# Performance work log

Hardware: AMD Instinct MI355X
Metric: run time of the kernel (lower is better)

## Reference

```python
import jax, jax.numpy as jnp
import numpy as np

B, N, D, P = 512, 64, 256, 512   # graphs, nodes/graph, feat dim, pairs/graph
DEG = 16
E = B * N * DEG                  # 524288 edges
H = 512                          # classifier hidden dim
LR_OUT, CR_OUT, MR_OUT = 4, 6, 17


def setup_inputs() -> dict:
    key = jax.random.key(0)
    ks = jax.random.split(key, 20)
    x = jax.random.normal(ks[0], (B * N, D), jnp.float32)
    # edges stay within each graph, as in a collated batch of graphs
    offs_e = jnp.repeat(jnp.arange(B, dtype=jnp.int32) * N, N * DEG)
    src = jax.random.randint(ks[1], (E,), 0, N, dtype=jnp.int32) + offs_e
    dst = jax.random.randint(ks[2], (E,), 0, N, dtype=jnp.int32) + offs_e
    edge_index = jnp.stack([src, dst])
    pairs = jax.random.randint(ks[3], (B, P, 2), 0, N, dtype=jnp.int32)
    s = 0.02
    inp = {
        'x': x, 'edge_index': edge_index, 'pairs': pairs,
        'gcn_w1': jax.random.normal(ks[4], (D, D), jnp.float32) * s,
        'gcn_b1': jnp.zeros((D,), jnp.float32),
        'gcn_w2': jax.random.normal(ks[5], (D, D), jnp.float32) * s,
        'gcn_b2': jnp.zeros((D,), jnp.float32),
        'lr_w1': jax.random.normal(ks[6], (D, H), jnp.float32) * s,
        'lr_b1': jnp.zeros((H,), jnp.float32),
        'lr_w2': jax.random.normal(ks[7], (H, LR_OUT), jnp.float32) * s,
        'lr_b2': jnp.zeros((LR_OUT,), jnp.float32),
        'cr_w1': jax.random.normal(ks[8], (D, H), jnp.float32) * s,
        'cr_b1': jnp.zeros((H,), jnp.float32),
        'cr_w2': jax.random.normal(ks[9], (H, CR_OUT), jnp.float32) * s,
        'cr_b2': jnp.zeros((CR_OUT,), jnp.float32),
        'mr_w1': jax.random.normal(ks[10], (D, H), jnp.float32) * s,
        'mr_b1': jnp.zeros((H,), jnp.float32),
        'mr_w2': jax.random.normal(ks[11], (H, MR_OUT), jnp.float32) * s,
        'mr_b2': jnp.zeros((MR_OUT,), jnp.float32),
    }
    return inp


def _gcn(x, src, dst, gcn_w1, gcn_b1, gcn_w2, gcn_b2):
    # vanilla GCN with self-loops and symmetric normalization
    n_tot = x.shape[0]
    loops = jnp.arange(n_tot, dtype=src.dtype)
    s = jnp.concatenate([src, loops])
    d = jnp.concatenate([dst, loops])
    deg = jax.ops.segment_sum(jnp.ones_like(s, dtype=x.dtype), d, num_segments=n_tot)
    norm = jax.lax.rsqrt(deg[s] * deg[d])  # [E + n_tot]

    def layer(h, W, b, act):
        m = jax.ops.segment_sum(h[s] * norm[:, None], d, num_segments=n_tot)
        o = m @ W + b
        return jax.nn.relu(o) if act else o

    h = layer(x, gcn_w1, gcn_b1, True)
    return layer(h, gcn_w2, gcn_b2, False)


def _mlp(z, w1, b1, w2, b2):
    return jax.nn.relu(z @ w1 + b1) @ w2 + b2


def reference(x, edge_index, pairs,
              gcn_w1, gcn_b1, gcn_w2, gcn_b2,
              lr_w1, lr_b1, lr_w2, lr_b2,
              cr_w1, cr_b1, cr_w2, cr_b2,
              mr_w1, mr_b1, mr_w2, mr_b2):
    emb = _gcn(x, edge_index[0], edge_index[1], gcn_w1, gcn_b1, gcn_w2, gcn_b2)  # [B*N, D]
    # decollate + batched pair gather (replaces the python double loop)
    offs = (jnp.arange(B, dtype=pairs.dtype) * N)[:, None, None]  # [B,1,1]
    gp = pairs + offs                                            # global node ids [B,P,2]
    e0 = emb[gp[..., 0].reshape(-1)].reshape(B, P, D)
    e1 = emb[gp[..., 1].reshape(-1)].reshape(B, P, D)
    ci = 0.5 * (e0 + e1)  # aggregate(emb0, emb1, 'mean')
    lr = _mlp(ci, lr_w1, lr_b1, lr_w2, lr_b2)
    cr = _mlp(ci, cr_w1, cr_b1, cr_w2, cr_b2)
    mr = _mlp(ci, mr_w1, mr_b1, mr_w2, mr_b2)
    return (lr, cr, mr)
```

## Files before the change

kernel.cpp:

```cpp
#include <hip/hip_runtime.h>
#include <hip/hip_bf16.h>

typedef __bf16 bf16x8 __attribute__((ext_vector_type(8)));
typedef __bf16 bf16x4 __attribute__((ext_vector_type(4)));
typedef float f32x16 __attribute__((ext_vector_type(16)));
typedef unsigned short u16x8 __attribute__((ext_vector_type(8)));
typedef unsigned int u32x4 __attribute__((ext_vector_type(4)));

#define E_EDGES 524288
#define OUT_CR_OFF 1048576
#define OUT_MR_OFF 2621440

static __device__ __forceinline__ float bf2f_(unsigned short u) {
  unsigned int x = ((unsigned int)u) << 16;
  return __builtin_bit_cast(float, x);
}
static __device__ __forceinline__ unsigned short f2bf_(float f) {
  return __builtin_bit_cast(unsigned short, (__bf16)f);
}
static __device__ __forceinline__ unsigned int pack2_(float a, float b) {
  return ((unsigned int)f2bf_(b) << 16) | (unsigned int)f2bf_(a);
}

__global__ void pack_weights(const float* __restrict__ lw1, const float* __restrict__ cw1,
                             const float* __restrict__ mw1,
                             const float* __restrict__ lw2, const float* __restrict__ cw2,
                             const float* __restrict__ mw2,
                             unsigned short* __restrict__ w1tp,
                             unsigned short* __restrict__ w2tp) {
  int idx = blockIdx.x * 256 + threadIdx.x;
  const int n1 = 3 * 16 * 32 * 32 * 8;
  if (idx < n1) {
    int h = idx >> 17;
    int rem = idx & 131071;
    int t = rem >> 13;
    int rem2 = rem & 8191;
    int kc = rem2 >> 8;
    int rem3 = rem2 & 255;
    int hidl = rem3 >> 3;
    int j = rem3 & 7;
    const float* w1 = (h == 0) ? lw1 : (h == 1) ? cw1 : mw1;
    w1tp[idx] = f2bf_(w1[(kc * 8 + j) * 512 + t * 32 + hidl]);
  } else {
    int i2 = idx - n1;
    if (i2 < 3 * 64 * 32 * 8) {
      int h = i2 >> 14;
      int rem = i2 & 16383;
      int kc = rem >> 8;
      int rem2 = rem & 255;
      int o = rem2 >> 3;
      int j = rem2 & 7;
      const float* w2 = (h == 0) ? lw2 : (h == 1) ? cw2 : mw2;
      int OUTD = (h == 0) ? 4 : (h == 1) ? 6 : 17;
      w2tp[i2] = (o < OUTD) ? f2bf_(w2[(kc * 8 + j) * OUTD + o]) : (unsigned short)0;
    }
  }
}

template <bool PACKED>
__launch_bounds__(512, 2)
__global__ void fused_gcn_heads(
    const float* __restrict__ x,
    const int* __restrict__ esrc, const int* __restrict__ edst,
    const int* __restrict__ pairs,
    const float* __restrict__ gw1, const float* __restrict__ gb1,
    const float* __restrict__ gw2, const float* __restrict__ gb2,
    const float* __restrict__ lw1, const float* __restrict__ lb1,
    const float* __restrict__ lw2, const float* __restrict__ lb2,
    const float* __restrict__ cw1, const float* __restrict__ cb1,
    const float* __restrict__ cw2, const float* __restrict__ cb2,
    const float* __restrict__ mw1, const float* __restrict__ mb1,
    const float* __restrict__ mw2, const float* __restrict__ mb2,
    const unsigned short* __restrict__ w1tp,
    const unsigned short* __restrict__ w2tp,
    float* __restrict__ out) {
  __shared__ unsigned short bufM[64 * 256];
  __shared__ __align__(16) unsigned short w1tile[8192];
  __shared__ __align__(16) unsigned short w2tile[1024];
  __shared__ float b1s[512];
  __shared__ __align__(16) short eS[1024], eD[1024];
  __shared__ short csr[1024];
  __shared__ int csroff[65];
  __shared__ float invdeg[64], rdeg[64];

  const int b = blockIdx.x, tid = threadIdx.x;
  const int wv = tid >> 6, lane = tid & 63;

  {
    const float4* xg = (const float4*)(x + b * (64 * 256));
    for (int i = tid; i < 4096; i += 512) {
      float4 v = xg[i];
      ushort4 o;
      o.x = f2bf_(v.x); o.y = f2bf_(v.y); o.z = f2bf_(v.z); o.w = f2bf_(v.w);
      *(ushort4*)&bufM[i * 4] = o;
    }
    const int eb = b * 1024, nb = b * 64;
    for (int i = tid; i < 1024; i += 512) {
      eS[i] = (short)(esrc[eb + i] - nb);
      eD[i] = (short)(edst[eb + i] - nb);
    }
  }
  __syncthreads();

  if (tid < 64) {
    const short n = (short)tid;
    int cnt = 0;
    for (int c = 0; c < 128; ++c) {
      const u16x8 dv = *(const u16x8*)&eD[c * 8];
#pragma unroll
      for (int j = 0; j < 8; ++j) cnt += ((short)dv[j] == n) ? 1 : 0;
    }
    int val = cnt;
#pragma unroll
    for (int off = 1; off < 64; off <<= 1) {
      int up = __shfl_up(val, off, 64);
      if (tid >= off) val += up;
    }
    csroff[tid] = val - cnt;
    if (tid == 63) csroff[64] = val;
    const float dg = (float)(cnt + 1);
    invdeg[tid] = 1.0f / dg;
    rdeg[tid] = rsqrtf(dg);
    int pos = val - cnt;
    for (int c = 0; c < 128; ++c) {
      const u16x8 dv = *(const u16x8*)&eD[c * 8];
      const u16x8 sv = *(const u16x8*)&eS[c * 8];
#pragma unroll
      for (int j = 0; j < 8; ++j)
        if ((short)dv[j] == n) csr[pos++] = (short)sv[j];
    }
  }
  __syncthreads();

  float4 acc[8];

  auto do_agg = [&]() {
#pragma unroll
    for (int k = 0; k < 8; ++k) {
      const int n = wv * 8 + k;
      const ushort4 xv = *(const ushort4*)&bufM[n * 256 + lane * 4];
      const float sd = invdeg[n];
      float ax = bf2f_(xv.x) * sd, ay = bf2f_(xv.y) * sd;
      float az = bf2f_(xv.z) * sd, aw = bf2f_(xv.w) * sd;
      const float rn = rdeg[n];
      const int eb0 = csroff[n], eb1 = csroff[n + 1];
      for (int e = eb0; e < eb1; ++e) {
        const int s = csr[e];
        const float wgt = rn * rdeg[s];
        const ushort4 sv = *(const ushort4*)&bufM[s * 256 + lane * 4];
        ax += bf2f_(sv.x) * wgt; ay += bf2f_(sv.y) * wgt;
        az += bf2f_(sv.z) * wgt; aw += bf2f_(sv.w) * wgt;
      }
      acc[k].x = ax; acc[k].y = ay; acc[k].z = az; acc[k].w = aw;
    }
  };

  auto writeback = [&]() {
#pragma unroll
    for (int k = 0; k < 8; ++k) {
      const int n = wv * 8 + k;
      ushort4 o;
      o.x = f2bf_(acc[k].x); o.y = f2bf_(acc[k].y);
      o.z = f2bf_(acc[k].z); o.w = f2bf_(acc[k].w);
      *(ushort4*)&bufM[n * 256 + lane * 4] = o;
    }
  };

  auto do_matmul = [&](const float* __restrict__ W, const float* __restrict__ bias,
                       bool relu) {
#pragma unroll
    for (int k = 0; k < 8; ++k) { acc[k].x = 0.f; acc[k].y = 0.f; acc[k].z = 0.f; acc[k].w = 0.f; }
    for (int d0 = 0; d0 < 256; d0 += 8) {
      float4 wr[8];
#pragma unroll
      for (int r = 0; r < 8; ++r) wr[r] = ((const float4*)(W + (d0 + r) * 256))[lane];
#pragma unroll
      for (int k = 0; k < 8; ++k) {
        const int n = wv * 8 + k;
        const u16x8 m8 = *(const u16x8*)&bufM[n * 256 + d0];
#pragma unroll
        for (int r = 0; r < 8; ++r) {
          const float s = bf2f_(m8[r]);
          acc[k].x += wr[r].x * s; acc[k].y += wr[r].y * s;
          acc[k].z += wr[r].z * s; acc[k].w += wr[r].w * s;
        }
      }
    }
    const float4 bb = ((const float4*)bias)[lane];
#pragma unroll
    for (int k = 0; k < 8; ++k) {
      acc[k].x += bb.x; acc[k].y += bb.y; acc[k].z += bb.z; acc[k].w += bb.w;
      if (relu) {
        acc[k].x = fmaxf(acc[k].x, 0.f); acc[k].y = fmaxf(acc[k].y, 0.f);
        acc[k].z = fmaxf(acc[k].z, 0.f); acc[k].w = fmaxf(acc[k].w, 0.f);
      }
    }
  };

  do_agg();
  __syncthreads(); writeback(); __syncthreads();
  do_matmul(gw1, gb1, true);
  __syncthreads(); writeback(); __syncthreads();
  do_agg();
  __syncthreads(); writeback(); __syncthreads();
  do_matmul(gw2, gb2, false);
  __syncthreads(); writeback(); __syncthreads();

  const int half = lane >> 5, ln = lane & 31;

  bf16x8 ci[2][16];
#pragma unroll
  for (int pg = 0; pg < 2; ++pg) {
    const int p = wv * 64 + pg * 32 + ln;
    const int2 pr = ((const int2*)pairs)[b * 512 + p];
    const unsigned short* e0 = &bufM[pr.x * 256];
    const unsigned short* e1 = &bufM[pr.y * 256];
#pragma unroll
    for (int s = 0; s < 16; ++s) {
      const int ko = s * 16 + half * 8;
      const u16x8 r0 = *(const u16x8*)(e0 + ko);
      const u16x8 r1 = *(const u16x8*)(e1 + ko);
      bf16x8 v;
#pragma unroll
      for (int j = 0; j < 8; ++j) v[j] = (__bf16)(0.5f * (bf2f_(r0[j]) + bf2f_(r1[j])));
      ci[pg][s] = v;
    }
  }

  for (int h = 0; h < 3; ++h) {
    const float* w1p = (h == 0) ? lw1 : (h == 1) ? cw1 : mw1;
    const float* w2p = (h == 0) ? lw2 : (h == 1) ? cw2 : mw2;
    const float* b1p = (h == 0) ? lb1 : (h == 1) ? cb1 : mb1;
    const float* b2p = (h == 0) ? lb2 : (h == 1) ? cb2 : mb2;
    const int OUTD = (h == 0) ? 4 : (h == 1) ? 6 : 17;
    float* outp = out + ((h == 0) ? 0 : (h == 1) ? OUT_CR_OFF : OUT_MR_OFF);

    __syncthreads();
    b1s[tid] = b1p[tid];

    f32x16 acc2[2];
#pragma unroll
    for (int i = 0; i < 16; ++i) { acc2[0][i] = 0.f; acc2[1][i] = 0.f; }

    for (int t = 0; t < 16; ++t) {
      __syncthreads();
      if (PACKED) {
        const float4* g1 = ((const float4*)w1tp) + (h * 16 + t) * 1024;
        float4* d1 = (float4*)w1tile;
        d1[tid] = g1[tid];
        d1[tid + 512] = g1[tid + 512];
        if (tid < 128)
          ((float4*)w2tile)[tid] = ((const float4*)w2tp)[(h * 64 + t * 4) * 32 + tid];
      } else {
        const int hidl = tid & 31, kc2 = tid >> 5;
#pragma unroll
        for (int r = 0; r < 2; ++r) {
          const int kc = kc2 * 2 + r;
          bf16x8 v;
#pragma unroll
          for (int j = 0; j < 8; ++j)
            v[j] = (__bf16)w1p[(kc * 8 + j) * 512 + t * 32 + hidl];
          *(bf16x8*)&w1tile[(kc * 32 + hidl) * 8] = v;
        }
        if (tid < 256) {
          const int q = tid >> 6, rem = tid & 63, o = rem >> 1, jh = rem & 1;
          bf16x4 v;
#pragma unroll
          for (int jj = 0; jj < 4; ++jj) {
            const int row = (t * 4 + q) * 8 + jh * 4 + jj;
            v[jj] = (o < OUTD) ? (__bf16)w2p[row * OUTD + o] : (__bf16)0.f;
          }
          *(bf16x4*)&w2tile[(q * 32 + o) * 8 + jh * 4] = v;
        }
      }
      __syncthreads();

#pragma unroll
      for (int pg = 0; pg < 2; ++pg) {
        f32x16 acc1;
#pragma unroll
        for (int i = 0; i < 16; ++i) acc1[i] = 0.f;
#pragma unroll
        for (int s = 0; s < 16; ++s) {
          const bf16x8 a = *(const bf16x8*)&w1tile[((2 * s + half) * 32 + ln) * 8];
          acc1 = __builtin_amdgcn_mfma_f32_32x32x16_bf16(a, ci[pg][s], acc1, 0, 0, 0);
        }
        float hv[16];
#pragma unroll
        for (int i = 0; i < 16; ++i) {
          const int row = (i & 3) + 8 * (i >> 2) + 4 * half;
          hv[i] = fmaxf(acc1[i] + b1s[t * 32 + row], 0.f);
        }
#pragma unroll
        for (int ks = 0; ks < 2; ++ks) {
          const int bse = ks * 8;
          const unsigned x0 = pack2_(hv[bse + 0], hv[bse + 1]);
          const unsigned x1 = pack2_(hv[bse + 2], hv[bse + 3]);
          const unsigned y0 = pack2_(hv[bse + 4], hv[bse + 5]);
          const unsigned y1 = pack2_(hv[bse + 6], hv[bse + 7]);
          const unsigned px0 = __shfl_xor(x0, 32);
          const unsigned px1 = __shfl_xor(x1, 32);
          const unsigned py0 = __shfl_xor(y0, 32);
          const unsigned py1 = __shfl_xor(y1, 32);
          u32x4 wt;
          wt[0] = half ? py0 : x0;
          wt[1] = half ? py1 : x1;
          wt[2] = half ? y0 : px0;
          wt[3] = half ? y1 : px1;
          const bf16x8 bfrag = __builtin_bit_cast(bf16x8, wt);
          const bf16x8 a2 = *(const bf16x8*)&w2tile[((ks * 2 + half) * 32 + ln) * 8];
          acc2[pg] = __builtin_amdgcn_mfma_f32_32x32x16_bf16(a2, bfrag, acc2[pg], 0, 0, 0);
        }
      }
    }

#pragma unroll
    for (int pg = 0; pg < 2; ++pg) {
      const int p = wv * 64 + pg * 32 + ln;
      const long q = (long)b * 512 + p;
#pragma unroll
      for (int g4 = 0; g4 < 4; ++g4) {
        const int o0 = g4 * 8 + 4 * half;
#pragma unroll
        for (int e = 0; e < 4; ++e) {
          const int o = o0 + e;
          if (o < OUTD) outp[q * OUTD + o] = acc2[pg][g4 * 4 + e] + b2p[o];
        }
      }
    }
  }
}

extern "C" void kernel_launch(void* const* d_in, const int* in_sizes, int n_in,
                              void* d_out, int out_size, void* d_ws, size_t ws_size,
                              hipStream_t stream) {
  (void)in_sizes; (void)n_in; (void)out_size;
  const float* x   = (const float*)d_in[0];
  const int* eidx  = (const int*)d_in[1];
  const int* pairs = (const int*)d_in[2];
  const float* gw1 = (const float*)d_in[3];
  const float* gb1 = (const float*)d_in[4];
  const float* gw2 = (const float*)d_in[5];
  const float* gb2 = (const float*)d_in[6];
  const float* lw1 = (const float*)d_in[7];
  const float* lb1 = (const float*)d_in[8];
  const float* lw2 = (const float*)d_in[9];
  const float* lb2 = (const float*)d_in[10];
  const float* cw1 = (const float*)d_in[11];
  const float* cb1 = (const float*)d_in[12];
  const float* cw2 = (const float*)d_in[13];
  const float* cb2 = (const float*)d_in[14];
  const float* mw1 = (const float*)d_in[15];
  const float* mb1 = (const float*)d_in[16];
  const float* mw2 = (const float*)d_in[17];
  const float* mb2 = (const float*)d_in[18];

  const size_t NEED = (size_t)(3 * 16 * 32 * 32 * 8 + 3 * 64 * 32 * 8) * 2;
  unsigned short* w1tp = (unsigned short*)d_ws;
  unsigned short* w2tp = w1tp + 3 * 16 * 32 * 32 * 8;

  if (d_ws != nullptr && ws_size >= NEED) {
    pack_weights<<<1728, 256, 0, stream>>>(lw1, cw1, mw1, lw2, cw2, mw2, w1tp, w2tp);
    fused_gcn_heads<true><<<512, 512, 0, stream>>>(
        x, eidx, eidx + E_EDGES, pairs, gw1, gb1, gw2, gb2,
        lw1, lb1, lw2, lb2, cw1, cb1, cw2, cb2, mw1, mb1, mw2, mb2,
        w1tp, w2tp, (float*)d_out);
  } else {
    fused_gcn_heads<false><<<512, 512, 0, stream>>>(
        x, eidx, eidx + E_EDGES, pairs, gw1, gb1, gw2, gb2,
        lw1, lb1, lw2, lb2, cw1, cb1, cw2, cb2, mw1, mb1, mw2, mb2,
        w1tp, w2tp, (float*)d_out);
  }
}
```

Baseline: 509.4 us.

## Use MFMA for GCN matmuls, swizzle LDS, double-buffer head weight tiles

The two GCN layer matmuls move from scalar FP32 FMA loops over global weights to bf16 MFMA, using a new pre-packed GCN weight layout in the workspace. Node features in LDS are stored with an XOR swizzle to reduce bank conflicts. The head MLP loop is flattened over all 48 head/tile steps, with a double-buffered LDS weight tile whose global loads are issued before the current tile's compute, and one barrier per step. Adds an LDS union and setprio hints; the GCN matmul now rounds weights to bf16, a precision change.

```diff
diff --git a/kernel.cpp b/kernel.cpp
--- a/kernel.cpp
+++ b/kernel.cpp
@@ -10,6 +10,9 @@
 #define E_EDGES 524288
 #define OUT_CR_OFF 1048576
 #define OUT_MR_OFF 2621440
+#define W1TP_ELEMS (48 * 9216)
+#define GCNW_ELEMS (2 * 8 * 16 * 64 * 8)
+#define WS_NEED ((size_t)(W1TP_ELEMS + GCNW_ELEMS) * 2)
 
 static __device__ __forceinline__ float bf2f_(unsigned short u) {
   unsigned int x = ((unsigned int)u) << 16;
@@ -22,37 +25,38 @@
   return ((unsigned int)f2bf_(b) << 16) | (unsigned int)f2bf_(a);
 }
 
-__global__ void pack_weights(const float* __restrict__ lw1, const float* __restrict__ cw1,
+__global__ void pack_weights(const float* __restrict__ gw1, const float* __restrict__ gw2,
+                             const float* __restrict__ lw1, const float* __restrict__ cw1,
                              const float* __restrict__ mw1,
                              const float* __restrict__ lw2, const float* __restrict__ cw2,
                              const float* __restrict__ mw2,
                              unsigned short* __restrict__ w1tp,
-                             unsigned short* __restrict__ w2tp) {
-  int idx = blockIdx.x * 256 + threadIdx.x;
-  const int n1 = 3 * 16 * 32 * 32 * 8;
-  if (idx < n1) {
-    int h = idx >> 17;
-    int rem = idx & 131071;
-    int t = rem >> 13;
-    int rem2 = rem & 8191;
-    int kc = rem2 >> 8;
-    int rem3 = rem2 & 255;
-    int hidl = rem3 >> 3;
-    int j = rem3 & 7;
-    const float* w1 = (h == 0) ? lw1 : (h == 1) ? cw1 : mw1;
-    w1tp[idx] = f2bf_(w1[(kc * 8 + j) * 512 + t * 32 + hidl]);
+                             unsigned short* __restrict__ gcnw) {
+  const int idx = blockIdx.x * 256 + threadIdx.x;
+  if (idx < W1TP_ELEMS) {
+    const int ht = idx / 9216;
+    const int r = idx - ht * 9216;
+    const int h = ht >> 4, tt = ht & 15;
+    if (r < 8192) {
+      const int kc = r >> 8, r2 = r & 255, hidl = r2 >> 3, j = r2 & 7;
+      const float* w1 = (h == 0) ? lw1 : (h == 1) ? cw1 : mw1;
+      w1tp[idx] = f2bf_(w1[(kc * 8 + j) * 512 + tt * 32 + hidl]);
+    } else {
+      const int r2 = r - 8192;
+      const int q = r2 >> 8, r3 = r2 & 255, o = r3 >> 3, j = r3 & 7;
+      const float* w2 = (h == 0) ? lw2 : (h == 1) ? cw2 : mw2;
+      const int OUTD = (h == 0) ? 4 : (h == 1) ? 6 : 17;
+      w1tp[idx] = (o < OUTD) ? f2bf_(w2[((tt * 4 + q) * 8 + j) * OUTD + o])
+                             : (unsigned short)0;
+    }
   } else {
-    int i2 = idx - n1;
-    if (i2 < 3 * 64 * 32 * 8) {
-      int h = i2 >> 14;
-      int rem = i2 & 16383;
-      int kc = rem >> 8;
-      int rem2 = rem & 255;
-      int o = rem2 >> 3;
-      int j = rem2 & 7;
-      const float* w2 = (h == 0) ? lw2 : (h == 1) ? cw2 : mw2;
-      int OUTD = (h == 0) ? 4 : (h == 1) ? 6 : 17;
-      w2tp[i2] = (o < OUTD) ? f2bf_(w2[(kc * 8 + j) * OUTD + o]) : (unsigned short)0;
+    const int g = idx - W1TP_ELEMS;
+    if (g < GCNW_ELEMS) {
+      const int layer = g >> 16, r = g & 65535;
+      const int O = r >> 13, r2 = r & 8191, s = r2 >> 9;
+      const int r3 = r2 & 511, lane = r3 >> 3, j = r3 & 7;
+      const float* W = layer ? gw2 : gw1;
+      gcnw[g] = f2bf_(W[(s * 16 + (lane >> 5) * 8 + j) * 256 + O * 32 + (lane & 31)]);
     }
   }
 }
@@ -72,32 +76,37 @@
     const float* __restrict__ mw1, const float* __restrict__ mb1,
     const float* __restrict__ mw2, const float* __restrict__ mb2,
     const unsigned short* __restrict__ w1tp,
-    const unsigned short* __restrict__ w2tp,
+    const unsigned short* __restrict__ gcnw,
     float* __restrict__ out) {
-  __shared__ unsigned short bufM[64 * 256];
-  __shared__ __align__(16) unsigned short w1tile[8192];
-  __shared__ __align__(16) unsigned short w2tile[1024];
-  __shared__ float b1s[512];
-  __shared__ __align__(16) short eS[1024], eD[1024];
-  __shared__ short csr[1024];
+  __shared__ unsigned short bufM[16384];
+  __shared__ union WU {
+    struct GG { short eS[1024]; short eD[1024]; short csr[1024]; } g;
+    unsigned short wbuf[2][9216];
+  } U;
   __shared__ int csroff[65];
   __shared__ float invdeg[64], rdeg[64];
+  __shared__ float b1s[1568];
 
   const int b = blockIdx.x, tid = threadIdx.x;
   const int wv = tid >> 6, lane = tid & 63;
+  const int half = lane >> 5, ln = lane & 31;
+
+  auto sidx = [](int node, int boff) {
+    return (node * 512 + (boff ^ ((node & 15) << 4))) >> 1;
+  };
 
   {
-    const float4* xg = (const float4*)(x + b * (64 * 256));
+    const float4* xg = (const float4*)(x + b * 16384);
     for (int i = tid; i < 4096; i += 512) {
-      float4 v = xg[i];
-      ushort4 o;
-      o.x = f2bf_(v.x); o.y = f2bf_(v.y); o.z = f2bf_(v.z); o.w = f2bf_(v.w);
-      *(ushort4*)&bufM[i * 4] = o;
+      const float4 v = xg[i];
+      ushort4 o4;
+      o4.x = f2bf_(v.x); o4.y = f2bf_(v.y); o4.z = f2bf_(v.z); o4.w = f2bf_(v.w);
+      *(ushort4*)&bufM[sidx(i >> 6, (i & 63) * 8)] = o4;
     }
     const int eb = b * 1024, nb = b * 64;
     for (int i = tid; i < 1024; i += 512) {
-      eS[i] = (short)(esrc[eb + i] - nb);
-      eD[i] = (short)(edst[eb + i] - nb);
+      U.g.eS[i] = (short)(esrc[eb + i] - nb);
+      U.g.eD[i] = (short)(edst[eb + i] - nb);
     }
   }
   __syncthreads();
@@ -106,14 +115,14 @@
     const short n = (short)tid;
     int cnt = 0;
     for (int c = 0; c < 128; ++c) {
-      const u16x8 dv = *(const u16x8*)&eD[c * 8];
+      const u16x8 dv = *(const u16x8*)&U.g.eD[c * 8];
 #pragma unroll
       for (int j = 0; j < 8; ++j) cnt += ((short)dv[j] == n) ? 1 : 0;
     }
     int val = cnt;
 #pragma unroll
     for (int off = 1; off < 64; off <<= 1) {
-      int up = __shfl_up(val, off, 64);
+      const int up = __shfl_up(val, off, 64);
       if (tid >= off) val += up;
     }
     csroff[tid] = val - cnt;
@@ -123,11 +132,11 @@
     rdeg[tid] = rsqrtf(dg);
     int pos = val - cnt;
     for (int c = 0; c < 128; ++c) {
-      const u16x8 dv = *(const u16x8*)&eD[c * 8];
-      const u16x8 sv = *(const u16x8*)&eS[c * 8];
+      const u16x8 dv = *(const u16x8*)&U.g.eD[c * 8];
+      const u16x8 sv = *(const u16x8*)&U.g.eS[c * 8];
 #pragma unroll
       for (int j = 0; j < 8; ++j)
-        if ((short)dv[j] == n) csr[pos++] = (short)sv[j];
+        if ((short)dv[j] == n) U.g.csr[pos++] = (short)sv[j];
     }
   }
   __syncthreads();
@@ -138,16 +147,16 @@
 #pragma unroll
     for (int k = 0; k < 8; ++k) {
       const int n = wv * 8 + k;
-      const ushort4 xv = *(const ushort4*)&bufM[n * 256 + lane * 4];
+      const ushort4 xv = *(const ushort4*)&bufM[sidx(n, lane * 8)];
       const float sd = invdeg[n];
       float ax = bf2f_(xv.x) * sd, ay = bf2f_(xv.y) * sd;
       float az = bf2f_(xv.z) * sd, aw = bf2f_(xv.w) * sd;
       const float rn = rdeg[n];
-      const int eb0 = csroff[n], eb1 = csroff[n + 1];
-      for (int e = eb0; e < eb1; ++e) {
-        const int s = csr[e];
+      const int e0 = csroff[n], e1 = csroff[n + 1];
+      for (int e = e0; e < e1; ++e) {
+        const int s = U.g.csr[e];
         const float wgt = rn * rdeg[s];
-        const ushort4 sv = *(const ushort4*)&bufM[s * 256 + lane * 4];
+        const ushort4 sv = *(const ushort4*)&bufM[sidx(s, lane * 8)];
         ax += bf2f_(sv.x) * wgt; ay += bf2f_(sv.y) * wgt;
         az += bf2f_(sv.z) * wgt; aw += bf2f_(sv.w) * wgt;
       }
@@ -159,67 +168,78 @@
 #pragma unroll
     for (int k = 0; k < 8; ++k) {
       const int n = wv * 8 + k;
-      ushort4 o;
-      o.x = f2bf_(acc[k].x); o.y = f2bf_(acc[k].y);
-      o.z = f2bf_(acc[k].z); o.w = f2bf_(acc[k].w);
-      *(ushort4*)&bufM[n * 256 + lane * 4] = o;
-    }
-  };
-
-  auto do_matmul = [&](const float* __restrict__ W, const float* __restrict__ bias,
-                       bool relu) {
-#pragma unroll
-    for (int k = 0; k < 8; ++k) { acc[k].x = 0.f; acc[k].y = 0.f; acc[k].z = 0.f; acc[k].w = 0.f; }
-    for (int d0 = 0; d0 < 256; d0 += 8) {
-      float4 wr[8];
-#pragma unroll
-      for (int r = 0; r < 8; ++r) wr[r] = ((const float4*)(W + (d0 + r) * 256))[lane];
-#pragma unroll
-      for (int k = 0; k < 8; ++k) {
-        const int n = wv * 8 + k;
-        const u16x8 m8 = *(const u16x8*)&bufM[n * 256 + d0];
-#pragma unroll
-        for (int r = 0; r < 8; ++r) {
-          const float s = bf2f_(m8[r]);
-          acc[k].x += wr[r].x * s; acc[k].y += wr[r].y * s;
-          acc[k].z += wr[r].z * s; acc[k].w += wr[r].w * s;
+      ushort4 o4;
+      o4.x = f2bf_(acc[k].x); o4.y = f2bf_(acc[k].y);
+      o4.z = f2bf_(acc[k].z); o4.w = f2bf_(acc[k].w);
+      *(ushort4*)&bufM[sidx(n, lane * 8)] = o4;
+    }
+  };
+
+  auto do_mm = [&](int layer, const float* __restrict__ Wg,
+                   const float* __restrict__ bias, bool relu) {
+    f32x16 a0, a1;
+#pragma unroll
+    for (int i = 0; i < 16; ++i) { a0[i] = 0.f; a1[i] = 0.f; }
+#pragma unroll
+    for (int s = 0; s < 16; ++s) {
+      bf16x8 aW;
+      if (PACKED) {
+        aW = *(const bf16x8*)&gcnw[(((layer * 8 + wv) * 16 + s) * 64 + lane) * 8];
+      } else {
+#pragma unroll
+        for (int j = 0; j < 8; ++j)
+          aW[j] = (__bf16)Wg[(s * 16 + half * 8 + j) * 256 + wv * 32 + ln];
+      }
+      const bf16x8 b0 = *(const bf16x8*)&bufM[sidx(ln, s * 32 + half * 16)];
+      const bf16x8 b1v = *(const bf16x8*)&bufM[sidx(32 + ln, s * 32 + half * 16)];
+      a0 = __builtin_amdgcn_mfma_f32_32x32x16_bf16(aW, b0, a0, 0, 0, 0);
+      a1 = __builtin_amdgcn_mfma_f32_32x32x16_bf16(aW, b1v, a1, 0, 0, 0);
+    }
+    __syncthreads();
+    float4 bb[4];
+#pragma unroll
+    for (int g4 = 0; g4 < 4; ++g4)
+      bb[g4] = *(const float4*)&bias[wv * 32 + g4 * 8 + 4 * half];
+#pragma unroll
+    for (int N = 0; N < 2; ++N) {
+      const int node = N * 32 + ln;
+#pragma unroll
+      for (int g4 = 0; g4 < 4; ++g4) {
+#pragma unroll
+        for (int e2 = 0; e2 < 2; ++e2) {
+          float v0 = (N ? a1 : a0)[g4 * 4 + e2 * 2 + 0] + bb[g4][e2 * 2 + 0];
+          float v1 = (N ? a1 : a0)[g4 * 4 + e2 * 2 + 1] + bb[g4][e2 * 2 + 1];
+          if (relu) { v0 = fmaxf(v0, 0.f); v1 = fmaxf(v1, 0.f); }
+          const int ocol = wv * 32 + g4 * 8 + 4 * half + e2 * 2;
+          *(unsigned int*)&bufM[sidx(node, ocol * 2)] = pack2_(v0, v1);
         }
       }
     }
-    const float4 bb = ((const float4*)bias)[lane];
-#pragma unroll
-    for (int k = 0; k < 8; ++k) {
-      acc[k].x += bb.x; acc[k].y += bb.y; acc[k].z += bb.z; acc[k].w += bb.w;
-      if (relu) {
-        acc[k].x = fmaxf(acc[k].x, 0.f); acc[k].y = fmaxf(acc[k].y, 0.f);
-        acc[k].z = fmaxf(acc[k].z, 0.f); acc[k].w = fmaxf(acc[k].w, 0.f);
-      }
-    }
-  };
-
-  do_agg();
-  __syncthreads(); writeback(); __syncthreads();
-  do_matmul(gw1, gb1, true);
-  __syncthreads(); writeback(); __syncthreads();
-  do_agg();
-  __syncthreads(); writeback(); __syncthreads();
-  do_matmul(gw2, gb2, false);
-  __syncthreads(); writeback(); __syncthreads();
-
-  const int half = lane >> 5, ln = lane & 31;
+    __syncthreads();
+  };
+
+  do_agg(); __syncthreads(); writeback(); __syncthreads();
+  do_mm(0, gw1, gb1, true);
+  do_agg(); __syncthreads(); writeback(); __syncthreads();
+  do_mm(1, gw2, gb2, false);
+
+  b1s[tid] = lb1[tid];
+  b1s[512 + tid] = cb1[tid];
+  b1s[1024 + tid] = mb1[tid];
+  if (tid < 4) b1s[1536 + tid] = lb2[tid];
+  else if (tid < 10) b1s[1536 + tid] = cb2[tid - 4];
+  else if (tid < 27) b1s[1536 + tid] = mb2[tid - 10];
 
   bf16x8 ci[2][16];
 #pragma unroll
   for (int pg = 0; pg < 2; ++pg) {
     const int p = wv * 64 + pg * 32 + ln;
     const int2 pr = ((const int2*)pairs)[b * 512 + p];
-    const unsigned short* e0 = &bufM[pr.x * 256];
-    const unsigned short* e1 = &bufM[pr.y * 256];
 #pragma unroll
     for (int s = 0; s < 16; ++s) {
-      const int ko = s * 16 + half * 8;
-      const u16x8 r0 = *(const u16x8*)(e0 + ko);
-      const u16x8 r1 = *(const u16x8*)(e1 + ko);
+      const int boff = s * 32 + half * 16;
+      const u16x8 r0 = *(const u16x8*)&bufM[sidx(pr.x, boff)];
+      const u16x8 r1 = *(const u16x8*)&bufM[sidx(pr.y, boff)];
       bf16x8 v;
 #pragma unroll
       for (int j = 0; j < 8; ++j) v[j] = (__bf16)(0.5f * (bf2f_(r0[j]) + bf2f_(r1[j])));
@@ -227,104 +247,140 @@
     }
   }
 
-  for (int h = 0; h < 3; ++h) {
-    const float* w1p = (h == 0) ? lw1 : (h == 1) ? cw1 : mw1;
-    const float* w2p = (h == 0) ? lw2 : (h == 1) ? cw2 : mw2;
-    const float* b1p = (h == 0) ? lb1 : (h == 1) ? cb1 : mb1;
-    const float* b2p = (h == 0) ? lb2 : (h == 1) ? cb2 : mb2;
-    const int OUTD = (h == 0) ? 4 : (h == 1) ? 6 : 17;
-    float* outp = out + ((h == 0) ? 0 : (h == 1) ? OUT_CR_OFF : OUT_MR_OFF);
-
+  float4 st0, st1, st2;
+  float w1r[16]; float w2r[4];
+  const int hidl = tid & 31, kc2 = tid >> 5;
+
+  auto stage_issue = [&](int ht) {
+    if (PACKED) {
+      const float4* g = (const float4*)(w1tp + ht * 9216);
+      st0 = g[tid]; st1 = g[tid + 512];
+      if (tid < 128) st2 = g[tid + 1024];
+    } else {
+      const int h = ht >> 4, tt = ht & 15;
+      const float* w1p = (h == 0) ? lw1 : (h == 1) ? cw1 : mw1;
+      const float* w2p = (h == 0) ? lw2 : (h == 1) ? cw2 : mw2;
+      const int OUTD = (h == 0) ? 4 : (h == 1) ? 6 : 17;
+#pragma unroll
+      for (int r = 0; r < 2; ++r)
+#pragma unroll
+        for (int j = 0; j < 8; ++j)
+          w1r[r * 8 + j] = w1p[((2 * kc2 + r) * 8 + j) * 512 + tt * 32 + hidl];
+      if (tid < 256) {
+        const int q4 = tid >> 6, rem = tid & 63, o = rem >> 1, jh = rem & 1;
+#pragma unroll
+        for (int jj = 0; jj < 4; ++jj) {
+          const int row = (tt * 4 + q4) * 8 + jh * 4 + jj;
+          w2r[jj] = (o < OUTD) ? w2p[row * OUTD + o] : 0.f;
+        }
+      }
+    }
+  };
+  auto stage_commit = [&](int bi) {
+    if (PACKED) {
+      float4* d = (float4*)U.wbuf[bi];
+      d[tid] = st0; d[tid + 512] = st1;
+      if (tid < 128) d[tid + 1024] = st2;
+    } else {
+#pragma unroll
+      for (int r = 0; r < 2; ++r) {
+        bf16x8 v;
+#pragma unroll
+        for (int j = 0; j < 8; ++j) v[j] = (__bf16)w1r[r * 8 + j];
+        *(bf16x8*)&U.wbuf[bi][((2 * kc2 + r) * 32 + hidl) * 8] = v;
+      }
+      if (tid < 256) {
+        const int q4 = tid >> 6, rem = tid & 63, o = rem >> 1, jh = rem & 1;
+        bf16x4 v4;
+#pragma unroll
+        for (int jj = 0; jj < 4; ++jj) v4[jj] = (__bf16)w2r[jj];
+        *(bf16x4*)&U.wbuf[bi][8192 + (q4 * 32 + o) * 8 + jh * 4] = v4;
+      }
+    }
+  };
+
+  stage_issue(0);
+  stage_commit(0);
+  __syncthreads();
+
+  f32x16 acc2_0, acc2_1;
+  for (int ht = 0; ht < 48; ++ht) {
+    const int h = ht >> 4, tt = ht & 15, cur = ht & 1;
+    if (tt == 0) {
+#pragma unroll
+      for (int i = 0; i < 16; ++i) { acc2_0[i] = 0.f; acc2_1[i] = 0.f; }
+    }
+    if (ht < 47) stage_issue(ht + 1);
+
+    f32x16 p0, p1;
+#pragma unroll
+    for (int i = 0; i < 16; ++i) { p0[i] = 0.f; p1[i] = 0.f; }
+    __builtin_amdgcn_s_setprio(1);
+#pragma unroll
+    for (int s = 0; s < 16; ++s) {
+      const bf16x8 a = *(const bf16x8*)&U.wbuf[cur][((2 * s + half) * 32 + ln) * 8];
+      p0 = __builtin_amdgcn_mfma_f32_32x32x16_bf16(a, ci[0][s], p0, 0, 0, 0);
+      p1 = __builtin_amdgcn_mfma_f32_32x32x16_bf16(a, ci[1][s], p1, 0, 0, 0);
+    }
+    __builtin_amdgcn_s_setprio(0);
+
+    const bf16x8 a2k0 = *(const bf16x8*)&U.wbuf[cur][8192 + ((0 + half) * 32 + ln) * 8];
+    const bf16x8 a2k1 = *(const bf16x8*)&U.wbuf[cur][8192 + ((2 + half) * 32 + ln) * 8];
+    float4 bb[4];
+#pragma unroll
+    for (int g4 = 0; g4 < 4; ++g4)
+      bb[g4] = *(const float4*)&b1s[h * 512 + tt * 32 + g4 * 8 + 4 * half];
+
+#pragma unroll
+    for (int pg = 0; pg < 2; ++pg) {
+      float hv[16];
+#pragma unroll
+      for (int i = 0; i < 16; ++i)
+        hv[i] = fmaxf((pg ? p1 : p0)[i] + bb[i >> 2][i & 3], 0.f);
+#pragma unroll
+      for (int ks = 0; ks < 2; ++ks) {
+        const int bse = ks * 8;
+        const unsigned x0 = pack2_(hv[bse + 0], hv[bse + 1]);
+        const unsigned x1 = pack2_(hv[bse + 2], hv[bse + 3]);
+        const unsigned y0 = pack2_(hv[bse + 4], hv[bse + 5]);
+        const unsigned y1 = pack2_(hv[bse + 6], hv[bse + 7]);
+        const unsigned px0 = __shfl_xor(x0, 32);
+        const unsigned px1 = __shfl_xor(x1, 32);
+        const unsigned py0 = __shfl_xor(y0, 32);
+        const unsigned py1 = __shfl_xor(y1, 32);
+        u32x4 wt;
+        wt[0] = half ? py0 : x0;
+        wt[1] = half ? py1 : x1;
+        wt[2] = half ? y0 : px0;
+        wt[3] = half ? y1 : px1;
+        const bf16x8 bfrag = __builtin_bit_cast(bf16x8, wt);
+        if (pg == 0)
+          acc2_0 = __builtin_amdgcn_mfma_f32_32x32x16_bf16(ks ? a2k1 : a2k0, bfrag,
+                                                           acc2_0, 0, 0, 0);
+        else
+          acc2_1 = __builtin_amdgcn_mfma_f32_32x32x16_bf16(ks ? a2k1 : a2k0, bfrag,
+                                                           acc2_1, 0, 0, 0);
+      }
+    }
+
+    if (ht < 47) stage_commit(cur ^ 1);
     __syncthreads();
-    b1s[tid] = b1p[tid];
-
-    f32x16 acc2[2];
-#pragma unroll
-    for (int i = 0; i < 16; ++i) { acc2[0][i] = 0.f; acc2[1][i] = 0.f; }
-
-    for (int t = 0; t < 16; ++t) {
-      __syncthreads();
-      if (PACKED) {
-        const float4* g1 = ((const float4*)w1tp) + (h * 16 + t) * 1024;
-        float4* d1 = (float4*)w1tile;
-        d1[tid] = g1[tid];
-        d1[tid + 512] = g1[tid + 512];
-        if (tid < 128)
-          ((float4*)w2tile)[tid] = ((const float4*)w2tp)[(h * 64 + t * 4) * 32 + tid];
-      } else {
-        const int hidl = tid & 31, kc2 = tid >> 5;
-#pragma unroll
-        for (int r = 0; r < 2; ++r) {
-          const int kc = kc2 * 2 + r;
-          bf16x8 v;
-#pragma unroll
-          for (int j = 0; j < 8; ++j)
-            v[j] = (__bf16)w1p[(kc * 8 + j) * 512 + t * 32 + hidl];
-          *(bf16x8*)&w1tile[(kc * 32 + hidl) * 8] = v;
-        }
-        if (tid < 256) {
-          const int q = tid >> 6, rem = tid & 63, o = rem >> 1, jh = rem & 1;
-          bf16x4 v;
-#pragma unroll
-          for (int jj = 0; jj < 4; ++jj) {
-            const int row = (t * 4 + q) * 8 + jh * 4 + jj;
-            v[jj] = (o < OUTD) ? (__bf16)w2p[row * OUTD + o] : (__bf16)0.f;
+
+    if (tt == 15) {
+      const int OUTD = (h == 0) ? 4 : (h == 1) ? 6 : 17;
+      float* outp = out + ((h == 0) ? 0 : (h == 1) ? OUT_CR_OFF : OUT_MR_OFF);
+      const int b2o = (h == 0) ? 1536 : (h == 1) ? 1540 : 1546;
+#pragma unroll
+      for (int pg = 0; pg < 2; ++pg) {
+        const long qq = (long)b * 512 + wv * 64 + pg * 32 + ln;
+#pragma unroll
+        for (int g4 = 0; g4 < 4; ++g4) {
+#pragma unroll
+          for (int e = 0; e < 4; ++e) {
+            const int o = g4 * 8 + 4 * half + e;
+            if (o < OUTD)
+              outp[qq * OUTD + o] = (pg ? acc2_1 : acc2_0)[g4 * 4 + e] + b1s[b2o + o];
           }
-          *(bf16x4*)&w2tile[(q * 32 + o) * 8 + jh * 4] = v;
-        }
-      }
-      __syncthreads();
-
-#pragma unroll
-      for (int pg = 0; pg < 2; ++pg) {
-        f32x16 acc1;
-#pragma unroll
-        for (int i = 0; i < 16; ++i) acc1[i] = 0.f;
-#pragma unroll
-        for (int s = 0; s < 16; ++s) {
-          const bf16x8 a = *(const bf16x8*)&w1tile[((2 * s + half) * 32 + ln) * 8];
-          acc1 = __builtin_amdgcn_mfma_f32_32x32x16_bf16(a, ci[pg][s], acc1, 0, 0, 0);
-        }
-        float hv[16];
-#pragma unroll
-        for (int i = 0; i < 16; ++i) {
-          const int row = (i & 3) + 8 * (i >> 2) + 4 * half;
-          hv[i] = fmaxf(acc1[i] + b1s[t * 32 + row], 0.f);
-        }
-#pragma unroll
-        for (int ks = 0; ks < 2; ++ks) {
-          const int bse = ks * 8;
-          const unsigned x0 = pack2_(hv[bse + 0], hv[bse + 1]);
-          const unsigned x1 = pack2_(hv[bse + 2], hv[bse + 3]);
-          const unsigned y0 = pack2_(hv[bse + 4], hv[bse + 5]);
-          const unsigned y1 = pack2_(hv[bse + 6], hv[bse + 7]);
-          const unsigned px0 = __shfl_xor(x0, 32);
-          const unsigned px1 = __shfl_xor(x1, 32);
-          const unsigned py0 = __shfl_xor(y0, 32);
-          const unsigned py1 = __shfl_xor(y1, 32);
-          u32x4 wt;
-          wt[0] = half ? py0 : x0;
-          wt[1] = half ? py1 : x1;
-          wt[2] = half ? y0 : px0;
-          wt[3] = half ? y1 : px1;
-          const bf16x8 bfrag = __builtin_bit_cast(bf16x8, wt);
-          const bf16x8 a2 = *(const bf16x8*)&w2tile[((ks * 2 + half) * 32 + ln) * 8];
-          acc2[pg] = __builtin_amdgcn_mfma_f32_32x32x16_bf16(a2, bfrag, acc2[pg], 0, 0, 0);
-        }
-      }
-    }
-
-#pragma unroll
-    for (int pg = 0; pg < 2; ++pg) {
-      const int p = wv * 64 + pg * 32 + ln;
-      const long q = (long)b * 512 + p;
-#pragma unroll
-      for (int g4 = 0; g4 < 4; ++g4) {
-        const int o0 = g4 * 8 + 4 * half;
-#pragma unroll
-        for (int e = 0; e < 4; ++e) {
-          const int o = o0 + e;
-          if (o < OUTD) outp[q * OUTD + o] = acc2[pg][g4 * 4 + e] + b2p[o];
         }
       }
     }
@@ -355,20 +411,20 @@
   const float* mw2 = (const float*)d_in[17];
   const float* mb2 = (const float*)d_in[18];
 
-  const size_t NEED = (size_t)(3 * 16 * 32 * 32 * 8 + 3 * 64 * 32 * 8) * 2;
   unsigned short* w1tp = (unsigned short*)d_ws;
-  unsigned short* w2tp = w1tp + 3 * 16 * 32 * 32 * 8;
-
-  if (d_ws != nullptr && ws_size >= NEED) {
-    pack_weights<<<1728, 256, 0, stream>>>(lw1, cw1, mw1, lw2, cw2, mw2, w1tp, w2tp);
+  unsigned short* gcnw = w1tp + W1TP_ELEMS;
+
+  if (d_ws != nullptr && ws_size >= WS_NEED) {
+    pack_weights<<<2240, 256, 0, stream>>>(gw1, gw2, lw1, cw1, mw1, lw2, cw2, mw2,
+                                           w1tp, gcnw);
     fused_gcn_heads<true><<<512, 512, 0, stream>>>(
         x, eidx, eidx + E_EDGES, pairs, gw1, gb1, gw2, gb2,
         lw1, lb1, lw2, lb2, cw1, cb1, cw2, cb2, mw1, mb1, mw2, mb2,
-        w1tp, w2tp, (float*)d_out);
+        w1tp, gcnw, (float*)d_out);
   } else {
     fused_gcn_heads<false><<<512, 512, 0, stream>>>(
         x, eidx, eidx + E_EDGES, pairs, gw1, gb1, gw2, gb2,
         lw1, lb1, lw2, lb2, cw1, cb1, cw2, cb2, mw1, mb1, mw2, mb2,
-        w1tp, w2tp, (float*)d_out);
-  }
-}
+        w1tp, gcnw, (float*)d_out);
+  }
+}
```

Result: faster. 426.6 us (-16.3%).
